# Kernel tuning notes

Measured on AMD Instinct MI355X. Metric: run time of the kernel, lower is better.

The kernel has to match this reference:

```python
import jax, jax.numpy as jnp
import numpy as np

N = 50000      # nodes
F_IN = 256     # nfeat
HID = 64       # nhid (per-head, layer 1)
H = 4          # heads layer 1
OUT = 64       # nhid2 (layer 2, heads=1, concat=False)
E = 800000     # edges (self-loops appended in reference)
NEG_SLOPE = 0.2  # PyG GATConv default LeakyReLU slope


def setup_inputs() -> dict:
    key = jax.random.key(0)
    ks = jax.random.split(key, 10)
    x = jax.random.normal(ks[0], (N, F_IN), dtype=jnp.float32)
    adj = jax.random.randint(ks[1], (2, E), 0, N)
    s1 = 1.0 / np.sqrt(F_IN)
    s2 = 1.0 / np.sqrt(H * HID)
    W1 = (jax.random.normal(ks[2], (F_IN, H * HID), dtype=jnp.float32) * s1)
    att_src1 = jax.random.normal(ks[3], (H, HID), dtype=jnp.float32) * 0.1
    att_dst1 = jax.random.normal(ks[4], (H, HID), dtype=jnp.float32) * 0.1
    b1 = jnp.zeros((H * HID,), dtype=jnp.float32)
    W2 = (jax.random.normal(ks[5], (H * HID, OUT), dtype=jnp.float32) * s2)
    att_src2 = jax.random.normal(ks[6], (1, OUT), dtype=jnp.float32) * 0.1
    att_dst2 = jax.random.normal(ks[7], (1, OUT), dtype=jnp.float32) * 0.1
    b2 = jnp.zeros((OUT,), dtype=jnp.float32)
    return {"x": x, "adj": adj, "W1": W1, "att_src1": att_src1,
            "att_dst1": att_dst1, "b1": b1, "W2": W2, "att_src2": att_src2,
            "att_dst2": att_dst2, "b2": b2}


def _gat_conv(x, src, dst, W, a_src, a_dst, bias, heads, out_ch, concat):
    n = x.shape[0]
    h = (x @ W).reshape(n, heads, out_ch)                    # [N, H, C]
    alpha_src = jnp.einsum('nhc,hc->nh', h, a_src)           # [N, H]
    alpha_dst = jnp.einsum('nhc,hc->nh', h, a_dst)           # [N, H]
    alpha = jax.nn.leaky_relu(alpha_src[src] + alpha_dst[dst],
                              negative_slope=NEG_SLOPE)      # [E, H]
    # segment softmax over incoming edges of each dst node
    m = jax.ops.segment_max(alpha, dst, num_segments=n)      # [N, H]
    e = jnp.exp(alpha - m[dst])
    denom = jax.ops.segment_sum(e, dst, num_segments=n)      # [N, H]
    a = e / denom[dst]                                       # [E, H]
    msg = h[src] * a[:, :, None]                             # [E, H, C]
    out = jax.ops.segment_sum(msg, dst, num_segments=n)      # [N, H, C]
    if concat:
        out = out.reshape(n, heads * out_ch)
    else:
        out = out.mean(axis=1)
    return out + bias


def reference(x, adj, W1, att_src1, att_dst1, b1, W2, att_src2, att_dst2, b2):
    loops = jnp.arange(N, dtype=adj.dtype)
    src = jnp.concatenate([adj[0], loops])
    dst = jnp.concatenate([adj[1], loops])
    h = _gat_conv(x, src, dst, W1, att_src1, att_dst1, b1, H, HID, True)
    h = jax.nn.elu(h)
    out = _gat_conv(h, src, dst, W2, att_src2, att_dst2, b2, 1, OUT, False)
    return jax.nn.log_softmax(out, axis=1)
```

## Files before the change

kernel.cpp:

```cpp
#include <hip/hip_runtime.h>
#include <cstdint>
#include <cstddef>

#define NN    50000
#define EE    800000
#define SLOPE 0.2f
#define MT64  782
#define CAP   64

#define NBIN  196
#define DSH   8
#define PBLK  1024
#define EPB   782
#define BCAP  14
#define OCAP  8192
#define CASTB 20
#define BUCKB NBIN

typedef unsigned short ushortT;
typedef __attribute__((ext_vector_type(8))) short short8;
typedef __attribute__((ext_vector_type(4))) float floatx4;

__device__ __forceinline__ float lrelu(float x){ return x > 0.f ? x : SLOPE * x; }
__device__ __forceinline__ float eluf(float x){ return x > 0.f ? x : __expf(x) - 1.f; }
__device__ __forceinline__ ushortT f2b(float f){ unsigned u = __float_as_uint(f); u += 0x7fff + ((u >> 16) & 1); return (ushortT)(u >> 16); }
__device__ __forceinline__ float   b2f(ushortT b){ return __uint_as_float(((unsigned)b) << 16); }

__global__ __launch_bounds__(256, 3) void binCast_k(const int* __restrict__ srcA,
                                                    const int* __restrict__ dstA,
                                                    unsigned* __restrict__ binned,
                                                    ushortT* __restrict__ cnt2,
                                                    unsigned* __restrict__ ovf,
                                                    int* __restrict__ ovfcnt,
                                                    const float* __restrict__ W1,
                                                    const float* __restrict__ W2,
                                                    ushortT* __restrict__ W1T,
                                                    ushortT* __restrict__ W2T)
{
    __shared__ float    tile[64][65];
    __shared__ int      hist[NBIN];
    __shared__ unsigned lrec[NBIN][BCAP];

    const int tid = threadIdx.x;
    if (blockIdx.x < CASTB) {
        const int lr = tid >> 6;
        const int lc = tid & 63;
        if (blockIdx.x < 16) {
            const int tr = blockIdx.x >> 2, tc = blockIdx.x & 3;
            #pragma unroll
            for (int i = 0; i < 16; ++i) {
                int r = lr + i * 4;
                tile[r][lc] = W1[(size_t)(tr * 64 + r) * 256 + tc * 64 + lc];
            }
            __syncthreads();
            #pragma unroll
            for (int i = 0; i < 16; ++i) {
                int r = lr + i * 4;
                W1T[(size_t)(tc * 64 + r) * 256 + tr * 64 + lc] = f2b(tile[lc][r]);
            }
        } else {
            const int tk = blockIdx.x - 16;
            #pragma unroll
            for (int i = 0; i < 16; ++i) {
                int r = lr + i * 4;
                tile[r][lc] = W2[(size_t)(tk * 64 + r) * 64 + lc];
            }
            __syncthreads();
            #pragma unroll
            for (int i = 0; i < 16; ++i) {
                int r = lr + i * 4;
                W2T[(size_t)r * 256 + tk * 64 + lc] = f2b(tile[lc][r]);
            }
        }
        return;
    }

    const int blk = blockIdx.x - CASTB;
    for (int i = tid; i < NBIN; i += 256) hist[i] = 0;
    __syncthreads();

    const int e0 = blk * EPB;
    const int e1 = min(e0 + EPB, EE);
    for (int e = e0 + tid; e < e1; e += 256) {
        int s = srcA[e], d = dstA[e];
        int bin = d >> DSH;
        unsigned rec = ((unsigned)s << DSH) | (unsigned)(d & 255);
        int r = atomicAdd(&hist[bin], 1);
        if (r < BCAP) lrec[bin][r] = rec;
        else {
            int o = atomicAdd(ovfcnt, 1);
            if (o < OCAP) ovf[o] = ((unsigned)s << 16) | (unsigned)d;
        }
    }
    __syncthreads();

    for (int b = tid; b < NBIN; b += 256)
        cnt2[(size_t)blk * NBIN + b] = (ushortT)min(hist[b], BCAP);
    for (int sIdx = tid; sIdx < NBIN * BCAP; sIdx += 256) {
        int b = sIdx / BCAP;
        int i = sIdx - b * BCAP;
        if (i < min(hist[b], BCAP))
            binned[((size_t)blk * NBIN + b) * BCAP + i] = lrec[b][i];
    }
}

__global__ __launch_bounds__(256, 3) void gembucket_k(const float* __restrict__ x,
                                                      const ushortT* __restrict__ W1T,
                                                      const float* __restrict__ attS,
                                                      const float* __restrict__ attD,
                                                      ushortT* __restrict__ h1b,
                                                      float* __restrict__ asrc,
                                                      float* __restrict__ adst,
                                                      const unsigned* __restrict__ binned,
                                                      const ushortT* __restrict__ cnt2,
                                                      const unsigned* __restrict__ ovf,
                                                      const int* __restrict__ ovfcnt,
                                                      ushortT* __restrict__ esorted,
                                                      int* __restrict__ cnt)
{
    __shared__ ushortT c2[PBLK];
    __shared__ int     lcnt[256];
    __shared__ ushortT lbuck[256][CAP];

    const int tid = threadIdx.x;
    if (blockIdx.x < BUCKB) {
        const int b = blockIdx.x;
        lcnt[tid] = 0;
        for (int i = tid; i < PBLK; i += 256) c2[i] = cnt2[(size_t)i * NBIN + b];
        __syncthreads();

        for (int s0 = tid; s0 < PBLK * BCAP; s0 += 2048) {
            unsigned recs[8]; int ok[8];
            #pragma unroll
            for (int q = 0; q < 8; ++q) {
                int s = s0 + q * 256;
                int blk = s / BCAP;
                int i = s - blk * BCAP;
                ok[q] = (i < (int)c2[blk]);
                recs[q] = ok[q] ? binned[((size_t)blk * NBIN + b) * BCAP + i] : 0u;
            }
            #pragma unroll
            for (int q = 0; q < 8; ++q) {
                if (ok[q]) {
                    int dl = recs[q] & 255;
                    int r = atomicAdd(&lcnt[dl], 1);
                    if (r < CAP) lbuck[dl][r] = (ushortT)(recs[q] >> DSH);
                }
            }
        }

        int nov = *ovfcnt;
        nov = nov > OCAP ? OCAP : nov;
        for (int i = tid; i < nov; i += 256) {
            unsigned rec = ovf[i];
            int d = rec & 0xFFFF;
            if ((d >> DSH) == b) {
                int r = atomicAdd(&lcnt[d & 255], 1);
                if (r < CAP) lbuck[d & 255][r] = (ushortT)(rec >> 16);
            }
        }
        __syncthreads();

        const int nbase = b << DSH;
        {
            int n = nbase + tid;
            if (n < NN) cnt[n] = lcnt[tid];
        }
        unsigned* ed = (unsigned*)(esorted + (size_t)nbase * CAP);
        const unsigned* ls = (const unsigned*)(&lbuck[0][0]);
        for (int i = tid; i < 256 * (CAP / 2); i += 256) {
            if (nbase + (i >> 5) < NN) ed[i] = ls[i];
        }
        return;
    }

    const int w    = tid >> 6;
    const int lane = tid & 63;
    const int m16  = lane & 15;
    const int quad = lane >> 4;
    const int wr   = w >> 1;
    const int wc   = w & 1;
    const int gb   = blockIdx.x - BUCKB;
    const int rowbase = gb * 64 + wr * 32;
    const int colbase = wc * 128;

    const long r0 = min(rowbase + m16,      NN - 1);
    const long r1 = min(rowbase + 16 + m16, NN - 1);
    const float* a0p = x + r0 * 256 + quad * 8;
    const float* a1p = x + r1 * 256 + quad * 8;
    const ushortT* bp0 = W1T + (size_t)(colbase + m16) * 256 + quad * 8;

    floatx4 acc[2][8];
    #pragma unroll
    for (int i = 0; i < 2; ++i)
        #pragma unroll
        for (int j = 0; j < 8; ++j) acc[i][j] = (floatx4){0.f, 0.f, 0.f, 0.f};

    #pragma unroll
    for (int it = 0; it < 8; ++it) {
        const int k0 = it * 32;
        float4 fa00 = *(const float4*)(a0p + k0);
        float4 fa01 = *(const float4*)(a0p + k0 + 4);
        float4 fa10 = *(const float4*)(a1p + k0);
        float4 fa11 = *(const float4*)(a1p + k0 + 4);
        uint4 fb[8];
        #pragma unroll
        for (int j = 0; j < 8; ++j)
            fb[j] = *(const uint4*)(bp0 + (size_t)j * 16 * 256 + k0);

        ushortT a16[16];
        a16[0]=f2b(fa00.x); a16[1]=f2b(fa00.y); a16[2]=f2b(fa00.z); a16[3]=f2b(fa00.w);
        a16[4]=f2b(fa01.x); a16[5]=f2b(fa01.y); a16[6]=f2b(fa01.z); a16[7]=f2b(fa01.w);
        a16[8]=f2b(fa10.x); a16[9]=f2b(fa10.y); a16[10]=f2b(fa10.z); a16[11]=f2b(fa10.w);
        a16[12]=f2b(fa11.x); a16[13]=f2b(fa11.y); a16[14]=f2b(fa11.z); a16[15]=f2b(fa11.w);
        short8 af0 = *(short8*)(a16);
        short8 af1 = *(short8*)(a16 + 8);

        #pragma unroll
        for (int j = 0; j < 8; ++j) {
            short8 bf = *(short8*)(&fb[j]);
            acc[0][j] = __builtin_amdgcn_mfma_f32_16x16x32_bf16(af0, bf, acc[0][j], 0, 0, 0);
            acc[1][j] = __builtin_amdgcn_mfma_f32_16x16x32_bf16(af1, bf, acc[1][j], 0, 0, 0);
        }
    }

    float attSv[8], attDv[8];
    #pragma unroll
    for (int j = 0; j < 8; ++j) {
        attSv[j] = attS[colbase + j * 16 + m16];
        attDv[j] = attD[colbase + j * 16 + m16];
    }

    #pragma unroll
    for (int i = 0; i < 2; ++i) {
        #pragma unroll
        for (int r = 0; r < 4; ++r) {
            int row = rowbase + i * 16 + quad * 4 + r;
            bool ok = row < NN;
            if (ok) {
                #pragma unroll
                for (int j = 0; j < 8; ++j)
                    h1b[(size_t)row * 256 + colbase + j * 16 + m16] = f2b(acc[i][j][r]);
            }
            float d0 = 0.f, d1 = 0.f, e0 = 0.f, e1 = 0.f;
            #pragma unroll
            for (int jj = 0; jj < 4; ++jj) {
                d0 += acc[i][jj][r]     * attSv[jj];
                e0 += acc[i][jj][r]     * attDv[jj];
                d1 += acc[i][jj + 4][r] * attSv[jj + 4];
                e1 += acc[i][jj + 4][r] * attDv[jj + 4];
            }
            #pragma unroll
            for (int off = 1; off < 16; off <<= 1) {
                d0 += __shfl_xor(d0, off); e0 += __shfl_xor(e0, off);
                d1 += __shfl_xor(d1, off); e1 += __shfl_xor(e1, off);
            }
            if (ok && m16 == 0) {
                int hb = row * 4 + wc * 2;
                asrc[hb] = d0; asrc[hb + 1] = d1;
                adst[hb] = e0; adst[hb + 1] = e1;
            }
        }
    }
}

__global__ __launch_bounds__(256) void gemm2_k(const ushortT* __restrict__ a2b,
                                               const ushortT* __restrict__ W2T,
                                               const float* __restrict__ attS,
                                               const float* __restrict__ attD,
                                               ushortT* __restrict__ t2b,
                                               float* __restrict__ asrc,
                                               float* __restrict__ adst)
{
    const int tid  = threadIdx.x;
    const int w    = tid >> 6;
    const int lane = tid & 63;
    const int m16  = lane & 15;
    const int quad = lane >> 4;
    const int rowbase = blockIdx.x * 64 + w * 16;

    const long r0 = min(rowbase + m16, NN - 1);
    const ushortT* ap  = a2b + r0 * 256 + quad * 8;
    const ushortT* bp0 = W2T + (size_t)m16 * 256 + quad * 8;

    floatx4 acc[4];
    #pragma unroll
    for (int j = 0; j < 4; ++j) acc[j] = (floatx4){0.f, 0.f, 0.f, 0.f};

    #pragma unroll
    for (int it = 0; it < 8; ++it) {
        const int k0 = it * 32;
        uint4 fa = *(const uint4*)(ap + k0);
        uint4 fb[4];
        #pragma unroll
        for (int j = 0; j < 4; ++j)
            fb[j] = *(const uint4*)(bp0 + (size_t)j * 16 * 256 + k0);
        short8 af = *(short8*)(&fa);
        #pragma unroll
        for (int j = 0; j < 4; ++j) {
            short8 bf = *(short8*)(&fb[j]);
            acc[j] = __builtin_amdgcn_mfma_f32_16x16x32_bf16(af, bf, acc[j], 0, 0, 0);
        }
    }

    float attSv[4], attDv[4];
    #pragma unroll
    for (int j = 0; j < 4; ++j) {
        attSv[j] = attS[j * 16 + m16];
        attDv[j] = attD[j * 16 + m16];
    }

    #pragma unroll
    for (int r = 0; r < 4; ++r) {
        int row = rowbase + quad * 4 + r;
        bool ok = row < NN;
        if (ok) {
            #pragma unroll
            for (int j = 0; j < 4; ++j)
                t2b[(size_t)row * 64 + j * 16 + m16] = f2b(acc[j][r]);
        }
        float ds = 0.f, dd = 0.f;
        #pragma unroll
        for (int j = 0; j < 4; ++j) {
            ds += acc[j][r] * attSv[j];
            dd += acc[j][r] * attDv[j];
        }
        #pragma unroll
        for (int off = 1; off < 16; off <<= 1) {
            ds += __shfl_xor(ds, off);
            dd += __shfl_xor(dd, off);
        }
        if (ok && m16 == 0) {
            asrc[row] = ds;
            adst[row] = dd;
        }
    }
}

__global__ __launch_bounds__(256) void agg1_k(const ushortT* __restrict__ esorted,
                                              const int* __restrict__ cnt,
                                              const ushortT* __restrict__ h1b,
                                              const float* __restrict__ asrc,
                                              const float* __restrict__ adst,
                                              const float* __restrict__ b1,
                                              ushortT* __restrict__ a2b)
{
    __shared__ float pbuf[4][64][4];
    __shared__ int   sbuf[4][64];
    int w = threadIdx.x >> 6;
    int lane = threadIdx.x & 63;
    int n = blockIdx.x * 4 + w;
    if (n >= NN) return;
    int start = n * CAP;
    int deg = min(max(cnt[n], 0), CAP);
    float4 adv = *(const float4*)(adst + (size_t)n * 4);
    float4 asf = *(const float4*)(asrc + (size_t)n * 4);
    int h = lane >> 4;
    int c4 = lane * 4;

    float4 pself;
    pself.x = __expf(lrelu(asf.x + adv.x));
    pself.y = __expf(lrelu(asf.y + adv.y));
    pself.z = __expf(lrelu(asf.z + adv.z));
    pself.w = __expf(lrelu(asf.w + adv.w));
    float psh = (h < 2) ? (h == 0 ? pself.x : pself.y) : (h == 2 ? pself.z : pself.w);

    ushort4 hsv = *(const ushort4*)(h1b + (size_t)n * 256 + c4);
    float4 ac0 = make_float4(b2f(hsv.x) * psh, b2f(hsv.y) * psh, b2f(hsv.z) * psh, b2f(hsv.w) * psh);
    float4 ac1 = make_float4(0.f,0.f,0.f,0.f);
    float4 ac2 = make_float4(0.f,0.f,0.f,0.f);
    float4 ac3 = make_float4(0.f,0.f,0.f,0.f);
    float4 ssv = make_float4(0.f, 0.f, 0.f, 0.f);

    if (lane < deg) {
        int s = esorted[start + lane];
        float4 a = *(const float4*)(asrc + (size_t)s * 4);
        float4 pv;
        pv.x = __expf(lrelu(a.x + adv.x));
        pv.y = __expf(lrelu(a.y + adv.y));
        pv.z = __expf(lrelu(a.z + adv.z));
        pv.w = __expf(lrelu(a.w + adv.w));
        ssv = pv;
        *(float4*)(&pbuf[w][lane][0]) = pv;
        sbuf[w][lane] = s;
    } else {
        *(float4*)(&pbuf[w][lane][0]) = make_float4(0.f, 0.f, 0.f, 0.f);
        sbuf[w][lane] = 0;
    }
    __builtin_amdgcn_wave_barrier();

    int nb = (deg + 7) >> 3;
    ushort4 bufA[8], bufB[8];

#define LOADR(BUF, J0) { _Pragma("unroll") for (int q = 0; q < 8; ++q) { \
        int sq = sbuf[w][(J0) + q]; \
        BUF[q] = *(const ushort4*)(h1b + (size_t)sq * 256 + c4); } }
#define CONSR(BUF, J0) { _Pragma("unroll") for (int q = 0; q < 8; ++q) { \
        float p = pbuf[w][(J0) + q][h]; \
        float4* ac = (q & 3) == 0 ? &ac0 : (q & 3) == 1 ? &ac1 : (q & 3) == 2 ? &ac2 : &ac3; \
        ac->x += b2f(BUF[q].x) * p; ac->y += b2f(BUF[q].y) * p; \
        ac->z += b2f(BUF[q].z) * p; ac->w += b2f(BUF[q].w) * p; } }

    if (nb > 0) {
        LOADR(bufA, 0)
        #pragma unroll
        for (int b = 0; b < 8; ++b) {
            const int j0 = b << 3;
            if (b & 1) {
                if (b + 1 < nb) LOADR(bufA, j0 + 8)
                CONSR(bufB, j0)
            } else {
                if (b + 1 < nb) LOADR(bufB, j0 + 8)
                CONSR(bufA, j0)
            }
            if (b + 1 >= nb) break;
        }
    }
#undef LOADR
#undef CONSR

    #pragma unroll
    for (int off = 1; off < 64; off <<= 1) {
        ssv.x += __shfl_xor(ssv.x, off); ssv.y += __shfl_xor(ssv.y, off);
        ssv.z += __shfl_xor(ssv.z, off); ssv.w += __shfl_xor(ssv.w, off);
    }
    float ssh = (h < 2) ? (h == 0 ? ssv.x : ssv.y) : (h == 2 ? ssv.z : ssv.w);
    float rdh = 1.f / (ssh + psh);

    float4 bv = *(const float4*)(b1 + c4);
    ushort4 o;
    o.x = f2b(eluf((ac0.x + ac1.x + ac2.x + ac3.x) * rdh + bv.x));
    o.y = f2b(eluf((ac0.y + ac1.y + ac2.y + ac3.y) * rdh + bv.y));
    o.z = f2b(eluf((ac0.z + ac1.z + ac2.z + ac3.z) * rdh + bv.z));
    o.w = f2b(eluf((ac0.w + ac1.w + ac2.w + ac3.w) * rdh + bv.w));
    *(ushort4*)(a2b + (size_t)n * 256 + c4) = o;
}

__global__ __launch_bounds__(256) void agg2_k(const ushortT* __restrict__ esorted,
                                              const int* __restrict__ cnt,
                                              const ushortT* __restrict__ t2b,
                                              const float* __restrict__ asrc,
                                              const float* __restrict__ adst,
                                              const float* __restrict__ b2,
                                              float* __restrict__ out)
{
    __shared__ float pbuf[4][64];
    __shared__ int   sbuf[4][64];
    int w = threadIdx.x >> 6;
    int lane = threadIdx.x & 63;
    int n = blockIdx.x * 4 + w;
    if (n >= NN) return;
    int start = n * CAP;
    int deg = min(max(cnt[n], 0), CAP);
    float adv = adst[n];

    float pself = __expf(lrelu(asrc[n] + adv));
    float a0 = b2f(t2b[(size_t)n * 64 + lane]) * pself;
    float a1 = 0.f, a2 = 0.f, a3 = 0.f;
    float ss = 0.f;

    if (lane < deg) {
        int s = esorted[start + lane];
        float p = __expf(lrelu(asrc[s] + adv));
        ss = p;
        pbuf[w][lane] = p;
        sbuf[w][lane] = s;
    } else {
        pbuf[w][lane] = 0.f;
        sbuf[w][lane] = 0;
    }
    __builtin_amdgcn_wave_barrier();

    int nb = (deg + 7) >> 3;
    ushortT bufA[8], bufB[8];

#define LOADR2(BUF, J0) { _Pragma("unroll") for (int q = 0; q < 8; ++q) { \
        int sq = sbuf[w][(J0) + q]; \
        BUF[q] = t2b[(size_t)sq * 64 + lane]; } }
#define CONSR2(BUF, J0) { _Pragma("unroll") for (int q = 0; q < 8; ++q) { \
        float p = pbuf[w][(J0) + q]; \
        float* ac = (q & 3) == 0 ? &a0 : (q & 3) == 1 ? &a1 : (q & 3) == 2 ? &a2 : &a3; \
        *ac += b2f(BUF[q]) * p; } }

    if (nb > 0) {
        LOADR2(bufA, 0)
        #pragma unroll
        for (int b = 0; b < 8; ++b) {
            const int j0 = b << 3;
            if (b & 1) {
                if (b + 1 < nb) LOADR2(bufA, j0 + 8)
                CONSR2(bufB, j0)
            } else {
                if (b + 1 < nb) LOADR2(bufB, j0 + 8)
                CONSR2(bufA, j0)
            }
            if (b + 1 >= nb) break;
        }
    }
#undef LOADR2
#undef CONSR2

    #pragma unroll
    for (int off = 1; off < 64; off <<= 1) ss += __shfl_xor(ss, off);
    float v = (a0 + a1 + a2 + a3) / (ss + pself) + b2[lane];

    float m2 = v;
    #pragma unroll
    for (int off = 32; off; off >>= 1) m2 = fmaxf(m2, __shfl_xor(m2, off));
    float ex = __expf(v - m2);
    float sm = ex;
    #pragma unroll
    for (int off = 32; off; off >>= 1) sm += __shfl_xor(sm, off);
    out[(size_t)n * 64 + lane] = v - m2 - __logf(sm);
}

extern "C" void kernel_launch(void* const* d_in, const int* in_sizes, int n_in,
                              void* d_out, int out_size, void* d_ws, size_t ws_size,
                              hipStream_t stream)
{
    const float* x   = (const float*)d_in[0];
    const int*   adj = (const int*)  d_in[1];
    const float* W1  = (const float*)d_in[2];
    const float* as1 = (const float*)d_in[3];
    const float* ad1 = (const float*)d_in[4];
    const float* b1  = (const float*)d_in[5];
    const float* W2  = (const float*)d_in[6];
    const float* as2 = (const float*)d_in[7];
    const float* ad2 = (const float*)d_in[8];
    const float* b2  = (const float*)d_in[9];
    float* out = (float*)d_out;

    const size_t szH1b = (size_t)NN * 256 * 2;
    const size_t szT2b = (size_t)NN * 64 * 2;
    const size_t szA4  = (size_t)NN * 4 * 4;
    const size_t szA1  = (size_t)NN * 4;
    const size_t szE   = (size_t)NN * CAP * 2;
    const size_t szBin = (size_t)NBIN * PBLK * BCAP * 4;
    const size_t szC2  = (size_t)PBLK * NBIN * 2;

    char* p = (char*)d_ws;
    ushortT* h1b  = (ushortT*)p; p += szH1b;
    ushortT* a2b  = (ushortT*)p; p += szH1b;
    ushortT* t2b  = (ushortT*)p; p += szT2b;
    ushortT* W1T  = (ushortT*)p; p += 256 * 256 * 2;
    ushortT* W2T  = (ushortT*)p; p += 64 * 256 * 2;
    float* asrc1  = (float*)p; p += szA4;
    float* adst1  = (float*)p; p += szA4;
    float* asrc2  = (float*)p; p += szA1;
    float* adst2  = (float*)p; p += szA1;
    ushortT* esorted = (ushortT*)p; p += szE;
    int* cnt      = (int*)p; p += szA1;
    unsigned* binned = (unsigned*)p; p += szBin;
    ushortT* cnt2 = (ushortT*)p; p += szC2;
    unsigned* ovf = (unsigned*)p; p += (size_t)OCAP * 4;
    int* ovfcnt   = (int*)p; p += 64;

    const int nwb = (NN + 3) / 4;

    hipMemsetAsync(ovfcnt, 0, sizeof(int), stream);

    binCast_k<<<CASTB + PBLK, 256, 0, stream>>>(adj, adj + EE, binned, cnt2, ovf, ovfcnt,
                                                W1, W2, W1T, W2T);

    gembucket_k<<<BUCKB + MT64, 256, 0, stream>>>(x, W1T, as1, ad1, h1b, asrc1, adst1,
                                                  binned, cnt2, ovf, ovfcnt, esorted, cnt);

    agg1_k<<<nwb, 256, 0, stream>>>(esorted, cnt, h1b, asrc1, adst1, b1, a2b);
    gemm2_k<<<MT64, 256, 0, stream>>>(a2b, W2T, as2, ad2, t2b, asrc2, adst2);
    agg2_k<<<nwb, 256, 0, stream>>>(esorted, cnt, t2b, asrc2, adst2, b2, out);
}
```

Measured before the change: 267.1 us.

## Slice layer-1 features into 32-column planes and aggregate per slice

The GEMM1 epilogue now writes h1 as eight column slices of 32 bf16 values each, one plane per slice, instead of row-major 256-wide rows. Aggregation for layer 1 launches eight times as many blocks. Each wave handles one node for one slice, with 8 edges per iteration and 8 lanes per 64-byte row, so each slice plane (about 3.2 MB) can stay cache-resident across the random gathers. The costs are recomputing the softmax weights 8 times per node, smaller gathers per lane, dropping the explicit double-buffered prefetch, and a strided output store pattern.

```diff
diff --git a/kernel.cpp b/kernel.cpp
--- a/kernel.cpp
+++ b/kernel.cpp
@@ -16,6 +16,8 @@
 #define OCAP  8192
 #define CASTB 20
 #define BUCKB NBIN
+
+#define SLW   32
 
 typedef unsigned short ushortT;
 typedef __attribute__((ext_vector_type(8))) short short8;
@@ -239,8 +241,11 @@
             bool ok = row < NN;
             if (ok) {
                 #pragma unroll
-                for (int j = 0; j < 8; ++j)
-                    h1b[(size_t)row * 256 + colbase + j * 16 + m16] = f2b(acc[i][j][r]);
+                for (int j = 0; j < 8; ++j) {
+                    int sl = (colbase >> 5) + (j >> 1);
+                    int cc = ((j & 1) << 4) + m16;
+                    h1b[(size_t)sl * NN * SLW + (size_t)row * SLW + cc] = f2b(acc[i][j][r]);
+                }
             }
             float d0 = 0.f, d1 = 0.f, e0 = 0.f, e1 = 0.f;
             #pragma unroll
@@ -261,6 +266,70 @@
                 adst[hb] = e0; adst[hb + 1] = e1;
             }
         }
+    }
+}
+
+__global__ __launch_bounds__(256) void agg1_k(const ushortT* __restrict__ esorted,
+                                              const int* __restrict__ cnt,
+                                              const ushortT* __restrict__ h1b,
+                                              const float* __restrict__ asrc,
+                                              const float* __restrict__ adst,
+                                              const float* __restrict__ b1,
+                                              ushortT* __restrict__ a2b)
+{
+    const int slice = blockIdx.x & 7;
+    const int grp   = blockIdx.x >> 3;
+    const int wv    = threadIdx.x >> 6;
+    const int lane  = threadIdx.x & 63;
+    const int n     = grp * 4 + wv;
+    if (n >= NN) return;
+    const int h = slice >> 1;
+    const ushortT* hs = h1b + (size_t)slice * NN * SLW;
+
+    int deg = min(max(cnt[n], 0), CAP);
+    float adv = adst[(size_t)n * 4 + h];
+    float pself = __expf(lrelu(asrc[(size_t)n * 4 + h] + adv));
+
+    int   s_reg = 0;
+    float p_reg = 0.f;
+    if (lane < deg) {
+        s_reg = esorted[(size_t)n * CAP + lane];
+        p_reg = __expf(lrelu(asrc[(size_t)s_reg * 4 + h] + adv));
+    }
+    float ss = p_reg;
+    #pragma unroll
+    for (int off = 1; off < 64; off <<= 1) ss += __shfl_xor(ss, off);
+    float rdh = 1.f / (ss + pself);
+
+    float4 acc = make_float4(0.f, 0.f, 0.f, 0.f);
+    const int nb = (deg + 7) >> 3;
+    const int eg = lane >> 3;
+    const int cw = lane & 7;
+    for (int b = 0; b < nb; ++b) {
+        int e = b * 8 + eg;
+        int s = __shfl(s_reg, e);
+        float p = __shfl(p_reg, e);
+        ushort4 hv = *(const ushort4*)(hs + (size_t)s * SLW + cw * 4);
+        acc.x += b2f(hv.x) * p; acc.y += b2f(hv.y) * p;
+        acc.z += b2f(hv.z) * p; acc.w += b2f(hv.w) * p;
+    }
+    #pragma unroll
+    for (int off = 8; off < 64; off <<= 1) {
+        acc.x += __shfl_xor(acc.x, off); acc.y += __shfl_xor(acc.y, off);
+        acc.z += __shfl_xor(acc.z, off); acc.w += __shfl_xor(acc.w, off);
+    }
+
+    if (lane < 8) {
+        ushort4 hv = *(const ushort4*)(hs + (size_t)n * SLW + lane * 4);
+        acc.x += b2f(hv.x) * pself; acc.y += b2f(hv.y) * pself;
+        acc.z += b2f(hv.z) * pself; acc.w += b2f(hv.w) * pself;
+        float4 bv = *(const float4*)(b1 + slice * SLW + lane * 4);
+        ushort4 o;
+        o.x = f2b(eluf(acc.x * rdh + bv.x));
+        o.y = f2b(eluf(acc.y * rdh + bv.y));
+        o.z = f2b(eluf(acc.z * rdh + bv.z));
+        o.w = f2b(eluf(acc.w * rdh + bv.w));
+        *(ushort4*)(a2b + (size_t)n * 256 + slice * SLW + lane * 4) = o;
     }
 }
 
@@ -335,105 +404,6 @@
             adst[row] = dd;
         }
     }
-}
-
-__global__ __launch_bounds__(256) void agg1_k(const ushortT* __restrict__ esorted,
-                                              const int* __restrict__ cnt,
-                                              const ushortT* __restrict__ h1b,
-                                              const float* __restrict__ asrc,
-                                              const float* __restrict__ adst,
-                                              const float* __restrict__ b1,
-                                              ushortT* __restrict__ a2b)
-{
-    __shared__ float pbuf[4][64][4];
-    __shared__ int   sbuf[4][64];
-    int w = threadIdx.x >> 6;
-    int lane = threadIdx.x & 63;
-    int n = blockIdx.x * 4 + w;
-    if (n >= NN) return;
-    int start = n * CAP;
-    int deg = min(max(cnt[n], 0), CAP);
-    float4 adv = *(const float4*)(adst + (size_t)n * 4);
-    float4 asf = *(const float4*)(asrc + (size_t)n * 4);
-    int h = lane >> 4;
-    int c4 = lane * 4;
-
-    float4 pself;
-    pself.x = __expf(lrelu(asf.x + adv.x));
-    pself.y = __expf(lrelu(asf.y + adv.y));
-    pself.z = __expf(lrelu(asf.z + adv.z));
-    pself.w = __expf(lrelu(asf.w + adv.w));
-    float psh = (h < 2) ? (h == 0 ? pself.x : pself.y) : (h == 2 ? pself.z : pself.w);
-
-    ushort4 hsv = *(const ushort4*)(h1b + (size_t)n * 256 + c4);
-    float4 ac0 = make_float4(b2f(hsv.x) * psh, b2f(hsv.y) * psh, b2f(hsv.z) * psh, b2f(hsv.w) * psh);
-    float4 ac1 = make_float4(0.f,0.f,0.f,0.f);
-    float4 ac2 = make_float4(0.f,0.f,0.f,0.f);
-    float4 ac3 = make_float4(0.f,0.f,0.f,0.f);
-    float4 ssv = make_float4(0.f, 0.f, 0.f, 0.f);
-
-    if (lane < deg) {
-        int s = esorted[start + lane];
-        float4 a = *(const float4*)(asrc + (size_t)s * 4);
-        float4 pv;
-        pv.x = __expf(lrelu(a.x + adv.x));
-        pv.y = __expf(lrelu(a.y + adv.y));
-        pv.z = __expf(lrelu(a.z + adv.z));
-        pv.w = __expf(lrelu(a.w + adv.w));
-        ssv = pv;
-        *(float4*)(&pbuf[w][lane][0]) = pv;
-        sbuf[w][lane] = s;
-    } else {
-        *(float4*)(&pbuf[w][lane][0]) = make_float4(0.f, 0.f, 0.f, 0.f);
-        sbuf[w][lane] = 0;
-    }
-    __builtin_amdgcn_wave_barrier();
-
-    int nb = (deg + 7) >> 3;
-    ushort4 bufA[8], bufB[8];
-
-#define LOADR(BUF, J0) { _Pragma("unroll") for (int q = 0; q < 8; ++q) { \
-        int sq = sbuf[w][(J0) + q]; \
-        BUF[q] = *(const ushort4*)(h1b + (size_t)sq * 256 + c4); } }
-#define CONSR(BUF, J0) { _Pragma("unroll") for (int q = 0; q < 8; ++q) { \
-        float p = pbuf[w][(J0) + q][h]; \
-        float4* ac = (q & 3) == 0 ? &ac0 : (q & 3) == 1 ? &ac1 : (q & 3) == 2 ? &ac2 : &ac3; \
-        ac->x += b2f(BUF[q].x) * p; ac->y += b2f(BUF[q].y) * p; \
-        ac->z += b2f(BUF[q].z) * p; ac->w += b2f(BUF[q].w) * p; } }
-
-    if (nb > 0) {
-        LOADR(bufA, 0)
-        #pragma unroll
-        for (int b = 0; b < 8; ++b) {
-            const int j0 = b << 3;
-            if (b & 1) {
-                if (b + 1 < nb) LOADR(bufA, j0 + 8)
-                CONSR(bufB, j0)
-            } else {
-                if (b + 1 < nb) LOADR(bufB, j0 + 8)
-                CONSR(bufA, j0)
-            }
-            if (b + 1 >= nb) break;
-        }
-    }
-#undef LOADR
-#undef CONSR
-
-    #pragma unroll
-    for (int off = 1; off < 64; off <<= 1) {
-        ssv.x += __shfl_xor(ssv.x, off); ssv.y += __shfl_xor(ssv.y, off);
-        ssv.z += __shfl_xor(ssv.z, off); ssv.w += __shfl_xor(ssv.w, off);
-    }
-    float ssh = (h < 2) ? (h == 0 ? ssv.x : ssv.y) : (h == 2 ? ssv.z : ssv.w);
-    float rdh = 1.f / (ssh + psh);
-
-    float4 bv = *(const float4*)(b1 + c4);
-    ushort4 o;
-    o.x = f2b(eluf((ac0.x + ac1.x + ac2.x + ac3.x) * rdh + bv.x));
-    o.y = f2b(eluf((ac0.y + ac1.y + ac2.y + ac3.y) * rdh + bv.y));
-    o.z = f2b(eluf((ac0.z + ac1.z + ac2.z + ac3.z) * rdh + bv.z));
-    o.w = f2b(eluf((ac0.w + ac1.w + ac2.w + ac3.w) * rdh + bv.w));
-    *(ushort4*)(a2b + (size_t)n * 256 + c4) = o;
 }
 
 __global__ __launch_bounds__(256) void agg2_k(const ushortT* __restrict__ esorted,
@@ -565,7 +535,8 @@
     gembucket_k<<<BUCKB + MT64, 256, 0, stream>>>(x, W1T, as1, ad1, h1b, asrc1, adst1,
                                                   binned, cnt2, ovf, ovfcnt, esorted, cnt);
 
-    agg1_k<<<nwb, 256, 0, stream>>>(esorted, cnt, h1b, asrc1, adst1, b1, a2b);
+    agg1_k<<<nwb * 8, 256, 0, stream>>>(esorted, cnt, h1b, asrc1, adst1, b1, a2b);
+
     gemm2_k<<<MT64, 256, 0, stream>>>(a2b, W2T, as2, ad2, t2b, asrc2, adst2);
     agg2_k<<<nwb, 256, 0, stream>>>(esorted, cnt, t2b, asrc2, adst2, b2, out);
 }
```

Result: slower. 361.0 us (+35.1%).

## Fuse layer-2 linear transform and attention scores into layer-1 aggregation epilogue

Applied to the files above, without the earlier changes.

Removes the separate MFMA gemm2 kernel and the bf16 intermediate activation buffer. Each wave now multiplies its node's ELU output by W2, repacked into 4-row interleaved bf16, using lane shuffles, and writes t2b plus the layer-2 source/destination attention scores directly. This avoids a full write and reread of the N×256 intermediate and one launch. In exchange it adds scalar FMA and shuffle work to the aggregation kernel instead of using matrix cores.

```diff
diff --git a/kernel.cpp b/kernel.cpp
--- a/kernel.cpp
+++ b/kernel.cpp
@@ -35,7 +35,7 @@
                                                     const float* __restrict__ W1,
                                                     const float* __restrict__ W2,
                                                     ushortT* __restrict__ W1T,
-                                                    ushortT* __restrict__ W2T)
+                                                    ushortT* __restrict__ W2P)
 {
     __shared__ float    tile[64][65];
     __shared__ int      hist[NBIN];
@@ -43,9 +43,9 @@
 
     const int tid = threadIdx.x;
     if (blockIdx.x < CASTB) {
-        const int lr = tid >> 6;
-        const int lc = tid & 63;
         if (blockIdx.x < 16) {
+            const int lr = tid >> 6;
+            const int lc = tid & 63;
             const int tr = blockIdx.x >> 2, tc = blockIdx.x & 3;
             #pragma unroll
             for (int i = 0; i < 16; ++i) {
@@ -60,16 +60,15 @@
             }
         } else {
             const int tk = blockIdx.x - 16;
-            #pragma unroll
-            for (int i = 0; i < 16; ++i) {
-                int r = lr + i * 4;
-                tile[r][lc] = W2[(size_t)(tk * 64 + r) * 64 + lc];
-            }
-            __syncthreads();
-            #pragma unroll
-            for (int i = 0; i < 16; ++i) {
-                int r = lr + i * 4;
-                W2T[(size_t)r * 256 + tk * 64 + lc] = f2b(tile[lc][r]);
+            for (int p4 = tid; p4 < 1024; p4 += 256) {
+                int q = tk * 16 + (p4 >> 6);
+                int j = p4 & 63;
+                ushort4 o4;
+                o4.x = f2b(W2[(size_t)(4 * q + 0) * 64 + j]);
+                o4.y = f2b(W2[(size_t)(4 * q + 1) * 64 + j]);
+                o4.z = f2b(W2[(size_t)(4 * q + 2) * 64 + j]);
+                o4.w = f2b(W2[(size_t)(4 * q + 3) * 64 + j]);
+                *(ushort4*)(W2P + ((size_t)q * 64 + j) * 4) = o4;
             }
         }
         return;
@@ -264,86 +263,18 @@
     }
 }
 
-__global__ __launch_bounds__(256) void gemm2_k(const ushortT* __restrict__ a2b,
-                                               const ushortT* __restrict__ W2T,
-                                               const float* __restrict__ attS,
-                                               const float* __restrict__ attD,
-                                               ushortT* __restrict__ t2b,
-                                               float* __restrict__ asrc,
-                                               float* __restrict__ adst)
-{
-    const int tid  = threadIdx.x;
-    const int w    = tid >> 6;
-    const int lane = tid & 63;
-    const int m16  = lane & 15;
-    const int quad = lane >> 4;
-    const int rowbase = blockIdx.x * 64 + w * 16;
-
-    const long r0 = min(rowbase + m16, NN - 1);
-    const ushortT* ap  = a2b + r0 * 256 + quad * 8;
-    const ushortT* bp0 = W2T + (size_t)m16 * 256 + quad * 8;
-
-    floatx4 acc[4];
-    #pragma unroll
-    for (int j = 0; j < 4; ++j) acc[j] = (floatx4){0.f, 0.f, 0.f, 0.f};
-
-    #pragma unroll
-    for (int it = 0; it < 8; ++it) {
-        const int k0 = it * 32;
-        uint4 fa = *(const uint4*)(ap + k0);
-        uint4 fb[4];
-        #pragma unroll
-        for (int j = 0; j < 4; ++j)
-            fb[j] = *(const uint4*)(bp0 + (size_t)j * 16 * 256 + k0);
-        short8 af = *(short8*)(&fa);
-        #pragma unroll
-        for (int j = 0; j < 4; ++j) {
-            short8 bf = *(short8*)(&fb[j]);
-            acc[j] = __builtin_amdgcn_mfma_f32_16x16x32_bf16(af, bf, acc[j], 0, 0, 0);
-        }
-    }
-
-    float attSv[4], attDv[4];
-    #pragma unroll
-    for (int j = 0; j < 4; ++j) {
-        attSv[j] = attS[j * 16 + m16];
-        attDv[j] = attD[j * 16 + m16];
-    }
-
-    #pragma unroll
-    for (int r = 0; r < 4; ++r) {
-        int row = rowbase + quad * 4 + r;
-        bool ok = row < NN;
-        if (ok) {
-            #pragma unroll
-            for (int j = 0; j < 4; ++j)
-                t2b[(size_t)row * 64 + j * 16 + m16] = f2b(acc[j][r]);
-        }
-        float ds = 0.f, dd = 0.f;
-        #pragma unroll
-        for (int j = 0; j < 4; ++j) {
-            ds += acc[j][r] * attSv[j];
-            dd += acc[j][r] * attDv[j];
-        }
-        #pragma unroll
-        for (int off = 1; off < 16; off <<= 1) {
-            ds += __shfl_xor(ds, off);
-            dd += __shfl_xor(dd, off);
-        }
-        if (ok && m16 == 0) {
-            asrc[row] = ds;
-            adst[row] = dd;
-        }
-    }
-}
-
 __global__ __launch_bounds__(256) void agg1_k(const ushortT* __restrict__ esorted,
                                               const int* __restrict__ cnt,
                                               const ushortT* __restrict__ h1b,
                                               const float* __restrict__ asrc,
                                               const float* __restrict__ adst,
                                               const float* __restrict__ b1,
-                                              ushortT* __restrict__ a2b)
+                                              const ushortT* __restrict__ W2P,
+                                              const float* __restrict__ attS2,
+                                              const float* __restrict__ attD2,
+                                              ushortT* __restrict__ t2b,
+                                              float* __restrict__ asrc2,
+                                              float* __restrict__ adst2)
 {
     __shared__ float pbuf[4][64][4];
     __shared__ int   sbuf[4][64];
@@ -428,12 +359,34 @@
     float rdh = 1.f / (ssh + psh);
 
     float4 bv = *(const float4*)(b1 + c4);
-    ushort4 o;
-    o.x = f2b(eluf((ac0.x + ac1.x + ac2.x + ac3.x) * rdh + bv.x));
-    o.y = f2b(eluf((ac0.y + ac1.y + ac2.y + ac3.y) * rdh + bv.y));
-    o.z = f2b(eluf((ac0.z + ac1.z + ac2.z + ac3.z) * rdh + bv.z));
-    o.w = f2b(eluf((ac0.w + ac1.w + ac2.w + ac3.w) * rdh + bv.w));
-    *(ushort4*)(a2b + (size_t)n * 256 + c4) = o;
+    float f0 = eluf((ac0.x + ac1.x + ac2.x + ac3.x) * rdh + bv.x);
+    float f1 = eluf((ac0.y + ac1.y + ac2.y + ac3.y) * rdh + bv.y);
+    float f2 = eluf((ac0.z + ac1.z + ac2.z + ac3.z) * rdh + bv.z);
+    float f3 = eluf((ac0.w + ac1.w + ac2.w + ac3.w) * rdh + bv.w);
+
+    float acc2 = 0.f;
+    const ushortT* wp = W2P + (size_t)lane * 4;
+    #pragma unroll 8
+    for (int q = 0; q < 64; ++q) {
+        float b0 = __shfl(f0, q);
+        float bb1 = __shfl(f1, q);
+        float bb2 = __shfl(f2, q);
+        float bb3 = __shfl(f3, q);
+        ushort4 wv = *(const ushort4*)(wp + (size_t)q * 256);
+        acc2 += b2f(wv.x) * b0 + b2f(wv.y) * bb1 + b2f(wv.z) * bb2 + b2f(wv.w) * bb3;
+    }
+    t2b[(size_t)n * 64 + lane] = f2b(acc2);
+    float ds = acc2 * attS2[lane];
+    float dd = acc2 * attD2[lane];
+    #pragma unroll
+    for (int off = 1; off < 64; off <<= 1) {
+        ds += __shfl_xor(ds, off);
+        dd += __shfl_xor(dd, off);
+    }
+    if (lane == 0) {
+        asrc2[n] = ds;
+        adst2[n] = dd;
+    }
 }
 
 __global__ __launch_bounds__(256) void agg2_k(const ushortT* __restrict__ esorted,
@@ -540,10 +493,9 @@
 
     char* p = (char*)d_ws;
     ushortT* h1b  = (ushortT*)p; p += szH1b;
-    ushortT* a2b  = (ushortT*)p; p += szH1b;
     ushortT* t2b  = (ushortT*)p; p += szT2b;
     ushortT* W1T  = (ushortT*)p; p += 256 * 256 * 2;
-    ushortT* W2T  = (ushortT*)p; p += 64 * 256 * 2;
+    ushortT* W2P  = (ushortT*)p; p += 64 * 256 * 2;
     float* asrc1  = (float*)p; p += szA4;
     float* adst1  = (float*)p; p += szA4;
     float* asrc2  = (float*)p; p += szA1;
@@ -560,12 +512,13 @@
     hipMemsetAsync(ovfcnt, 0, sizeof(int), stream);
 
     binCast_k<<<CASTB + PBLK, 256, 0, stream>>>(adj, adj + EE, binned, cnt2, ovf, ovfcnt,
-                                                W1, W2, W1T, W2T);
+                                                W1, W2, W1T, W2P);
 
     gembucket_k<<<BUCKB + MT64, 256, 0, stream>>>(x, W1T, as1, ad1, h1b, asrc1, adst1,
                                                   binned, cnt2, ovf, ovfcnt, esorted, cnt);
 
-    agg1_k<<<nwb, 256, 0, stream>>>(esorted, cnt, h1b, asrc1, adst1, b1, a2b);
-    gemm2_k<<<MT64, 256, 0, stream>>>(a2b, W2T, as2, ad2, t2b, asrc2, adst2);
+    agg1_k<<<nwb, 256, 0, stream>>>(esorted, cnt, h1b, asrc1, adst1, b1,
+                                    W2P, as2, ad2, t2b, asrc2, adst2);
+
     agg2_k<<<nwb, 256, 0, stream>>>(esorted, cnt, t2b, asrc2, adst2, b2, out);
 }
```

Result: slower. 344.8 us (+29.1%).
